# Kernel tuning notes

Hardware: AMD Instinct MI355X
Metric: run time of the kernel (lower is better)

The kernel has to match this reference:

```python
import jax, jax.numpy as jnp
import numpy as np


def setup_inputs() -> dict:
    key = jax.random.key(0)
    k1, k2, k3 = jax.random.split(key, 3)
    bs, r, d = 4, 4096, 64
    G = jax.random.uniform(k1, (bs, d), dtype=jnp.float32)          # eigenvalues (non-negative)
    V = jax.random.normal(k2, (bs, r, d), dtype=jnp.float32)        # eigenvectors / spectral embedding
    weights = jax.random.uniform(k3, (1,), dtype=jnp.float32)       # learned scalar t
    return {"G": G, "V": V, "weights": weights}


def reference(G, V, weights):
    # Original: eVs = diag(max(G,0)^(2t)); y = E@eVs@Phi2^T + Phi2@eVs@E^T - 2*Phi@eVs@Phi^T
    # Since eVs is diagonal, this is the weighted pairwise squared distance:
    # y[b,i,j] = sum_k w[b,k] * (V[b,i,k] - V[b,j,k])^2 with w = max(G,0)^(2t).
    t = weights[0]
    w = jnp.maximum(G, jnp.zeros_like(G)) ** (2.0 * t)   # (bs, d)
    Vw = V * w[:, None, :]                               # (bs, r, d) elementwise diag scaling
    s = jnp.sum(Vw * V, axis=-1)                         # (bs, r): weighted squared norms
    cross = jnp.einsum('brd,bsd->brs', Vw, V)            # (bs, r, r)
    y = s[:, :, None] + s[:, None, :] - 2.0 * cross
    return y
```

## Files before the change

kernel.cpp:

```cpp
#include <hip/hip_runtime.h>
#include <hip/hip_bf16.h>


typedef __attribute__((ext_vector_type(8))) short bf16x8;
typedef __attribute__((ext_vector_type(4))) float f32x4;

constexpr int BS = 4, R = 4096, D = 64;
constexpr int LS = 260;

__global__ __launch_bounds__(256) void prep_kernel(
    const float* __restrict__ G, const float* __restrict__ V,
    const float* __restrict__ wt,
    __hip_bfloat16* __restrict__ u_bf, float* __restrict__ s)
{
    int row  = blockIdx.x * 4 + (threadIdx.x >> 6);
    int lane = threadIdx.x & 63;
    if (row >= BS * R) return;
    int b = row / R;

    float t  = wt[0];
    float g  = fmaxf(G[b * D + lane], 0.0f);
    float sw = powf(g, t);
    float u  = sw * V[(size_t)row * D + lane];

    __hip_bfloat16 ub = __float2bfloat16(u);
    u_bf[(size_t)row * D + lane] = ub;

    float uf   = __bfloat162float(ub);
    float prod = uf * uf;
    #pragma unroll
    for (int off = 32; off; off >>= 1) prod += __shfl_down(prod, off);
    if (lane == 0) s[row] = prod;
}

__global__ __launch_bounds__(512) void dist_kernel(
    const short* __restrict__ U, const float* __restrict__ s,
    float* __restrict__ out)
{
    __shared__ float lds[64 * LS];

    int lane = threadIdx.x & 63;
    int wave = threadIdx.x >> 6;
    int wr   = wave >> 2;
    int wc   = wave & 3;

    int b  = blockIdx.z;
    int jb = blockIdx.x * 256;
    int i0 = blockIdx.y * 128;

    const short* Ap = U + ((size_t)b * R + i0 + wr * 64) * D;
    const short* Bp = U + ((size_t)b * R + jb + wc * 64) * D;
    const float* sb = s + (size_t)b * R;

    int lrow = lane & 15;
    int kgrp = lane >> 4;

    bf16x8 a[4][2];
    #pragma unroll
    for (int rb = 0; rb < 4; ++rb)
        #pragma unroll
        for (int ks = 0; ks < 2; ++ks)
            a[rb][ks] = *(const bf16x8*)(Ap + (rb * 16 + lrow) * D + ks * 32 + kgrp * 8);

    f32x4 acc[4][4];
    #pragma unroll
    for (int rb = 0; rb < 4; ++rb)
        #pragma unroll
        for (int jt = 0; jt < 4; ++jt)
            acc[rb][jt] = f32x4{0.f, 0.f, 0.f, 0.f};

    #pragma unroll
    for (int jt = 0; jt < 4; ++jt) {
        const short* Bt = Bp + jt * 16 * D;
        bf16x8 b0 = *(const bf16x8*)(Bt + lrow * D +      kgrp * 8);
        bf16x8 b1 = *(const bf16x8*)(Bt + lrow * D + 32 + kgrp * 8);
        #pragma unroll
        for (int rb = 0; rb < 4; ++rb) {
            acc[rb][jt] = __builtin_amdgcn_mfma_f32_16x16x32_bf16(a[rb][0], b0, acc[rb][jt], 0, 0, 0);
            acc[rb][jt] = __builtin_amdgcn_mfma_f32_16x16x32_bf16(a[rb][1], b1, acc[rb][jt], 0, 0, 0);
        }
    }

    float si_lane = sb[i0 + wr * 64 + lane];

    float* outb = out + ((size_t)b * R + i0) * R + jb;

    #pragma unroll
    for (int c = 0; c < 2; ++c) {
        if (wr == c) {
            #pragma unroll
            for (int rb = 0; rb < 4; ++rb) {
                #pragma unroll
                for (int rg = 0; rg < 4; ++rg) {
                    int rl = rb * 16 + kgrp * 4 + rg;
                    float si = __shfl(si_lane, rl);
                    #pragma unroll
                    for (int jt = 0; jt < 4; ++jt) {
                        float sj = sb[jb + wc * 64 + jt * 16 + lrow];
                        float y  = si + sj - 2.0f * acc[rb][jt][rg];
                        lds[rl * LS + wc * 64 + jt * 16 + lrow] = y;
                    }
                }
            }
        }
        __syncthreads();

        #pragma unroll
        for (int r = 0; r < 8; ++r) {
            int rl = wave * 8 + r;
            f32x4 v = *(const f32x4*)&lds[rl * LS + lane * 4];
            __builtin_nontemporal_store(v,
                (f32x4*)(outb + (size_t)(c * 64 + rl) * R + lane * 4));
        }
        if (c == 0) __syncthreads();
    }
}

extern "C" void kernel_launch(void* const* d_in, const int* in_sizes, int n_in,
                              void* d_out, int out_size, void* d_ws, size_t ws_size,
                              hipStream_t stream) {
    const float* G  = (const float*)d_in[0];
    const float* V  = (const float*)d_in[1];
    const float* wt = (const float*)d_in[2];
    float* out = (float*)d_out;

    char* ws = (char*)d_ws;
    __hip_bfloat16* u_bf = (__hip_bfloat16*)ws;
    float*          s    = (float*)        (ws + (size_t)BS * R * D * 2);

    prep_kernel<<<BS * R / 4, 256, 0, stream>>>(G, V, wt, u_bf, s);

    dim3 grid(R / 256, R / 128, BS);
    dist_kernel<<<grid, 512, 0, stream>>>((const short*)u_bf, s, out);
}
```

Baseline: 65.09 us.

## Switch to 32x32 MFMA tiles and store output directly without LDS staging

Each wave now computes a 32x128 tile with 32x32x16 bf16 MFMAs instead of a 64x64 tile with 16x16x32 MFMAs. The LDS transpose buffer and the __syncthreads barriers are removed, so results are written straight from the accumulators with scalar nontemporal stores. The launch bounds gain an occupancy hint of 4. The stores are now 4-byte per lane, 128 bytes contiguous per half-wave, instead of 16-byte vector stores that covered full rows. That may hurt write efficiency in this store-bound kernel.

Result: slower. 77.65 us (+19.3%).

```diff
diff --git a/kernel.cpp b/kernel.cpp
--- a/kernel.cpp
+++ b/kernel.cpp
@@ -2,11 +2,10 @@
 #include <hip/hip_bf16.h>
 
 
-typedef __attribute__((ext_vector_type(8))) short bf16x8;
-typedef __attribute__((ext_vector_type(4))) float f32x4;
+typedef __attribute__((ext_vector_type(8)))  short bf16x8;
+typedef __attribute__((ext_vector_type(16))) float f32x16;
 
 constexpr int BS = 4, R = 4096, D = 64;
-constexpr int LS = 260;
 
 __global__ __launch_bounds__(256) void prep_kernel(
     const float* __restrict__ G, const float* __restrict__ V,
@@ -33,86 +32,62 @@
     if (lane == 0) s[row] = prod;
 }
 
-__global__ __launch_bounds__(512) void dist_kernel(
+__global__ __launch_bounds__(512, 4) void dist_kernel(
     const short* __restrict__ U, const float* __restrict__ s,
     float* __restrict__ out)
 {
-    __shared__ float lds[64 * LS];
-
     int lane = threadIdx.x & 63;
     int wave = threadIdx.x >> 6;
-    int wr   = wave >> 2;
-    int wc   = wave & 3;
+    int wr   = wave >> 1;
+    int wc   = wave & 1;
+    int half = lane >> 5;
+    int l31  = lane & 31;
 
     int b  = blockIdx.z;
     int jb = blockIdx.x * 256;
     int i0 = blockIdx.y * 128;
+    int iw = i0 + wr * 32;
+    int jw = jb + wc * 128;
 
-    const short* Ap = U + ((size_t)b * R + i0 + wr * 64) * D;
-    const short* Bp = U + ((size_t)b * R + jb + wc * 64) * D;
+    const short* Ap = U + ((size_t)b * R + iw) * D;
+    const short* Bp = U + ((size_t)b * R + jw) * D;
     const float* sb = s + (size_t)b * R;
 
-    int lrow = lane & 15;
-    int kgrp = lane >> 4;
+    bf16x8 a[4];
+    #pragma unroll
+    for (int ks = 0; ks < 4; ++ks)
+        a[ks] = *(const bf16x8*)(Ap + l31 * D + ks * 16 + half * 8);
 
-    bf16x8 a[4][2];
+    f32x16 acc[4];
     #pragma unroll
-    for (int rb = 0; rb < 4; ++rb)
+    for (int jt = 0; jt < 4; ++jt)
         #pragma unroll
-        for (int ks = 0; ks < 2; ++ks)
-            a[rb][ks] = *(const bf16x8*)(Ap + (rb * 16 + lrow) * D + ks * 32 + kgrp * 8);
-
-    f32x4 acc[4][4];
-    #pragma unroll
-    for (int rb = 0; rb < 4; ++rb)
-        #pragma unroll
-        for (int jt = 0; jt < 4; ++jt)
-            acc[rb][jt] = f32x4{0.f, 0.f, 0.f, 0.f};
+        for (int r = 0; r < 16; ++r) acc[jt][r] = 0.f;
 
     #pragma unroll
     for (int jt = 0; jt < 4; ++jt) {
-        const short* Bt = Bp + jt * 16 * D;
-        bf16x8 b0 = *(const bf16x8*)(Bt + lrow * D +      kgrp * 8);
-        bf16x8 b1 = *(const bf16x8*)(Bt + lrow * D + 32 + kgrp * 8);
+        const short* Bt = Bp + jt * 32 * D;
         #pragma unroll
-        for (int rb = 0; rb < 4; ++rb) {
-            acc[rb][jt] = __builtin_amdgcn_mfma_f32_16x16x32_bf16(a[rb][0], b0, acc[rb][jt], 0, 0, 0);
-            acc[rb][jt] = __builtin_amdgcn_mfma_f32_16x16x32_bf16(a[rb][1], b1, acc[rb][jt], 0, 0, 0);
+        for (int ks = 0; ks < 4; ++ks) {
+            bf16x8 bq = *(const bf16x8*)(Bt + l31 * D + ks * 16 + half * 8);
+            acc[jt] = __builtin_amdgcn_mfma_f32_32x32x16_bf16(a[ks], bq, acc[jt], 0, 0, 0);
         }
     }
 
-    float si_lane = sb[i0 + wr * 64 + lane];
-
-    float* outb = out + ((size_t)b * R + i0) * R + jb;
+    float si_lane = sb[iw + l31];
+    float* outb = out + ((size_t)b * R + iw) * R + jw;
 
     #pragma unroll
-    for (int c = 0; c < 2; ++c) {
-        if (wr == c) {
-            #pragma unroll
-            for (int rb = 0; rb < 4; ++rb) {
-                #pragma unroll
-                for (int rg = 0; rg < 4; ++rg) {
-                    int rl = rb * 16 + kgrp * 4 + rg;
-                    float si = __shfl(si_lane, rl);
-                    #pragma unroll
-                    for (int jt = 0; jt < 4; ++jt) {
-                        float sj = sb[jb + wc * 64 + jt * 16 + lrow];
-                        float y  = si + sj - 2.0f * acc[rb][jt][rg];
-                        lds[rl * LS + wc * 64 + jt * 16 + lrow] = y;
-                    }
-                }
-            }
+    for (int jt = 0; jt < 4; ++jt) {
+        float sj = sb[jw + jt * 32 + l31];
+        #pragma unroll
+        for (int r = 0; r < 16; ++r) {
+            int row  = (r & 3) + 8 * (r >> 2) + 4 * half;
+            float si = __shfl(si_lane, row);
+            float y  = si + sj - 2.0f * acc[jt][r];
+            __builtin_nontemporal_store(y,
+                outb + (size_t)row * R + jt * 32 + l31);
         }
-        __syncthreads();
-
-        #pragma unroll
-        for (int r = 0; r < 8; ++r) {
-            int rl = wave * 8 + r;
-            f32x4 v = *(const f32x4*)&lds[rl * LS + lane * 4];
-            __builtin_nontemporal_store(v,
-                (f32x4*)(outb + (size_t)(c * 64 + rl) * R + lane * 4));
-        }
-        if (c == 0) __syncthreads();
     }
 }
 
```
